# Performance work log

Hardware: AMD Instinct MI355X
Metric: run time of the kernel (lower is better)

## Reference

```python
import jax, jax.numpy as jnp
import numpy as np

NUM_HEADS = 8


def _forward(x, Wq, bq, Wk, bk, Wv, bv, Wo, bo, w1, b1, w2, b2, tau):
    B, S, E = x.shape
    H = NUM_HEADS
    hd = E // H
    scale = hd ** -0.5

    def heads(t):
        return t.reshape(B, S, H, hd).transpose(0, 2, 1, 3)  # [B,H,S,hd]

    q = heads(x @ Wq + bq)
    k = heads(x @ Wk + bk)
    v = heads(x @ Wv + bv)
    s = jnp.einsum('bhqd,bhkd->bhqk', q, k) * scale  # [B,H,S,S]

    # ---- autopoietic transform (vectorized over batch, no mask) ----
    s = jnp.clip(jnp.nan_to_num(s, nan=0.0, posinf=10.0, neginf=-10.0), -15.0, 15.0)
    ma = s.mean(axis=1)  # mean over heads -> [B,S,S]
    eps_safe = 0.05  # clamp(eps=1e-6, 0.05, 0.8)
    sa = jnp.clip(jnp.clip(ma, -8.0, 8.0) * eps_safe, -10.0, 10.0)
    # 1x1 conv on [1,1,S,S] == per-channel scalar scale+bias -> [B,C,S,S]
    hid = jax.nn.relu(jnp.clip(sa[:, None] * w1[None, :, None, None]
                               + b1[None, :, None, None], -5.0, 5.0))
    ap = jnp.clip(jnp.einsum('bcij,c->bij', hid, w2) + b2, -5.0, 5.0)
    taylor = jnp.clip(1.0 + 0.05 * (ap * 50.0), 0.5, 1.5)
    sig = jax.nn.sigmoid(taylor)
    p = jax.nn.softmax(jnp.clip(ma, -10.0, 10.0), axis=-1)
    Hent = -p * jnp.log(p + 1e-6)
    Fm = jax.nn.softmax(3.0 * Hent, axis=-1)
    t = sig * Fm
    eo = jnp.sqrt((ma * ma).sum(axis=(1, 2), keepdims=True)) + 1e-4  # fro norm
    et = jnp.sqrt((t * t).sum(axis=(1, 2), keepdims=True)) + 1e-4
    t = jnp.clip(eo / et, 0.8, 1.2) * t
    tm = t.mean(axis=(1, 2), keepdims=True)
    om = ma.mean(axis=(1, 2), keepdims=True)
    tstd = jnp.sqrt(jnp.clip(((t - tm) ** 2).mean(axis=(1, 2), keepdims=True), 0.01, None))
    ostd = jnp.sqrt(jnp.clip(((ma - om) ** 2).mean(axis=(1, 2), keepdims=True), 0.01, None))
    gd = jnp.clip(ostd / tstd, 0.8, 1.2)
    ar = jnp.clip(jnp.abs(ma).max(axis=(1, 2), keepdims=True), 1.0, 10.0)
    sm = jnp.clip(0.3 / jnp.log1p(ar), 0.1, 0.5)
    st = tm + sm * gd * (t - tm)  # scaled_transform
    ent = Hent.mean(axis=(1, 2), keepdims=True)
    ne = ent / jnp.log(jnp.float32(S))  # normalized entropy (max_entropy = log S)
    rr = 0.4 * (1.0 - jnp.clip(ne, 0.0, 0.4))  # residual ratio (base 0.4, entropy-damped)
    # blend transform back into per-head scores (res_scale = 1.0)
    s = s + rr[:, None] * (st - ma)[:, None]

    attn = jax.nn.softmax(s / tau, axis=-1)
    out = jnp.einsum('bhqk,bhkd->bhqd', attn, v)
    out = out.transpose(0, 2, 1, 3).reshape(B, S, E)
    return out @ Wo + bo


def setup_inputs() -> dict:
    key = jax.random.key(0)
    ks = jax.random.split(key, 8)
    B, S, E, C = 4, 512, 512, 128
    w_scale = 0.02
    return {
        'x': jax.random.normal(ks[0], (B, S, E), dtype=jnp.float32),
        'Wq': jax.random.normal(ks[1], (E, E), dtype=jnp.float32) * w_scale,
        'bq': jnp.zeros((E,), jnp.float32),
        'Wk': jax.random.normal(ks[2], (E, E), dtype=jnp.float32) * w_scale,
        'bk': jnp.zeros((E,), jnp.float32),
        'Wv': jax.random.normal(ks[3], (E, E), dtype=jnp.float32) * w_scale,
        'bv': jnp.zeros((E,), jnp.float32),
        'Wo': jax.random.normal(ks[4], (E, E), dtype=jnp.float32) * w_scale,
        'bo': jnp.zeros((E,), jnp.float32),
        'w1': jax.random.normal(ks[5], (C,), dtype=jnp.float32) * 0.5,
        'b1': jnp.zeros((C,), jnp.float32),
        'w2': jax.random.normal(ks[6], (C,), dtype=jnp.float32) * 0.1,
        'b2': jnp.zeros((1,), jnp.float32),
        'tau': jnp.ones((1,), jnp.float32),
    }


def reference(x, Wq, bq, Wk, bk, Wv, bv, Wo, bo, w1, b1, w2, b2, tau):
    return _forward(x, Wq, bq, Wk, bk, Wv, bv, Wo, bo, w1, b1, w2, b2, tau)
```

## Files before the change

### kernel.cpp

```cpp
#include <hip/hip_runtime.h>
#include <math.h>

#define BB 4
#define SS 512
#define EE 512
#define NH 8
#define HD 64
#define NC 128
#define NTAB 4096

typedef _Float16 f16x8 __attribute__((ext_vector_type(8)));
typedef float f32x4 __attribute__((ext_vector_type(4)));

struct HL { _Float16 h, l; };

__device__ __forceinline__ float clampf(float v, float lo, float hi) {
  return fminf(fmaxf(v, lo), hi);
}
__device__ __forceinline__ HL split16(float x) {
  HL r;
  r.h = (_Float16)x;
  r.l = (_Float16)(x - (float)r.h);
  return r;
}

__device__ __forceinline__ float waveRedSum(float v) {
#pragma unroll
  for (int o = 32; o; o >>= 1) v += __shfl_xor(v, o);
  return v;
}
__device__ __forceinline__ float waveRedMax(float v) {
#pragma unroll
  for (int o = 32; o; o >>= 1) v = fmaxf(v, __shfl_xor(v, o));
  return v;
}
__device__ __forceinline__ float blockRedSum8(float v, float* red) {
  int tid = threadIdx.x;
  v = waveRedSum(v);
  __syncthreads();
  if ((tid & 63) == 0) red[tid >> 6] = v;
  __syncthreads();
  float s = 0.f;
#pragma unroll
  for (int i = 0; i < 8; ++i) s += red[i];
  return s;
}
__device__ __forceinline__ float blockRedMax8(float v, float* red) {
  int tid = threadIdx.x;
  v = waveRedMax(v);
  __syncthreads();
  if ((tid & 63) == 0) red[tid >> 6] = v;
  __syncthreads();
  float s = red[0];
#pragma unroll
  for (int i = 1; i < 8; ++i) s = fmaxf(s, red[i]);
  return s;
}

__global__ __launch_bounds__(256) void k_prep(
    const float* __restrict__ Wq, const float* __restrict__ Wk,
    const float* __restrict__ Wv, const float* __restrict__ Wo,
    const float* __restrict__ x,
    _Float16* __restrict__ Wth, _Float16* __restrict__ Wtl,
    _Float16* __restrict__ xh) {
  const int j = blockIdx.x;
  const int tid = threadIdx.x;
  if (j >= 256) {
    const int rb = (j - 256) * 64;
    const int r = tid >> 2;
    const int c0 = (tid & 3) * 128;
    const float* src = x + (size_t)(rb + r) * EE + c0;
    _Float16* dst = xh + (size_t)(rb + r) * EE + c0;
#pragma unroll
    for (int c = 0; c < 128; c += 8) {
      float4 a = *(const float4*)(src + c);
      float4 b = *(const float4*)(src + c + 4);
      f16x8 h;
      h[0] = (_Float16)a.x; h[1] = (_Float16)a.y;
      h[2] = (_Float16)a.z; h[3] = (_Float16)a.w;
      h[4] = (_Float16)b.x; h[5] = (_Float16)b.y;
      h[6] = (_Float16)b.z; h[7] = (_Float16)b.w;
      *(f16x8*)(dst + c) = h;
    }
    return;
  }
  const int z = j >> 6;
  const int rem = j & 63;
  const int k0 = (rem & 7) * 64, n0 = (rem >> 3) * 64;
  const float* W = (z == 0) ? Wq : (z == 1) ? Wk : (z == 2) ? Wv : Wo;
  __shared__ float Tt[64][68];
  const int r = tid >> 2, c = (tid & 3) * 16;
#pragma unroll
  for (int jj = 0; jj < 16; jj += 4)
    *(float4*)&Tt[r][c + jj] =
        *(const float4*)(W + (size_t)(k0 + r) * EE + n0 + c + jj);
  __syncthreads();
  f16x8 h0, l0, h1, l1;
#pragma unroll
  for (int jj = 0; jj < 8; ++jj) {
    HL r0 = split16(Tt[c + jj][r]);
    HL r1 = split16(Tt[c + 8 + jj][r]);
    h0[jj] = r0.h; l0[jj] = r0.l;
    h1[jj] = r1.h; l1[jj] = r1.l;
  }
  _Float16* dh = Wth + ((size_t)z * EE + n0 + r) * EE + k0 + c;
  _Float16* dl = Wtl + ((size_t)z * EE + n0 + r) * EE + k0 + c;
  *(f16x8*)dh = h0;
  *(f16x8*)(dh + 8) = h1;
  *(f16x8*)dl = l0;
  *(f16x8*)(dl + 8) = l1;
}

__global__ __launch_bounds__(256) void k_qkv_mfma(
    const _Float16* __restrict__ xh,
    const _Float16* __restrict__ Wth, const _Float16* __restrict__ Wtl,
    const float* __restrict__ bq, const float* __restrict__ bk,
    const float* __restrict__ bv, const float* __restrict__ w1,
    const float* __restrict__ b1, const float* __restrict__ w2,
    const float* __restrict__ b2, float* __restrict__ T,
    _Float16* __restrict__ qh,
    _Float16* __restrict__ kh, _Float16* __restrict__ kl,
    _Float16* __restrict__ vth, _Float16* __restrict__ vtl) {
  const int which = blockIdx.z;
  const int tid = threadIdx.x;
  const int wave = tid >> 6, lane = tid & 63;
  const int quad = lane >> 4, l16 = lane & 15;
  const int m0 = blockIdx.y * 64;
  const int n0 = blockIdx.x * 64;
  const _Float16* Bh = Wth + (size_t)which * EE * EE;
  const _Float16* Bl = Wtl + (size_t)which * EE * EE;

  __shared__ __align__(16) char smpool[27648];
  _Float16(*LAh)[72] = (_Float16(*)[72])(smpool);
  _Float16(*LBh)[72] = (_Float16(*)[72])(smpool + 9216);
  _Float16(*LBl)[72] = (_Float16(*)[72])(smpool + 18432);
  float(*TR)[68] = (float(*)[68])(smpool);

  const int sr0 = tid >> 3, sc0 = (tid & 7) * 8;
  const int sr1 = sr0 + 32;

  f16x8 rA0h = *(const f16x8*)(xh + (size_t)(m0 + sr0) * EE + sc0);
  f16x8 rA1h = *(const f16x8*)(xh + (size_t)(m0 + sr1) * EE + sc0);
  f16x8 rB0h = *(const f16x8*)(Bh + (size_t)(n0 + sr0) * EE + sc0);
  f16x8 rB0l = *(const f16x8*)(Bl + (size_t)(n0 + sr0) * EE + sc0);
  f16x8 rB1h = *(const f16x8*)(Bh + (size_t)(n0 + sr1) * EE + sc0);
  f16x8 rB1l = *(const f16x8*)(Bl + (size_t)(n0 + sr1) * EE + sc0);

  f32x4 acc[4] = {};
  for (int k0 = 0; k0 < EE; k0 += 64) {
    if (k0) __syncthreads();
    *(f16x8*)&LAh[sr0][sc0] = rA0h;
    *(f16x8*)&LAh[sr1][sc0] = rA1h;
    *(f16x8*)&LBh[sr0][sc0] = rB0h;
    *(f16x8*)&LBl[sr0][sc0] = rB0l;
    *(f16x8*)&LBh[sr1][sc0] = rB1h;
    *(f16x8*)&LBl[sr1][sc0] = rB1l;
    __syncthreads();
    if (k0 + 64 < EE) {
      const int kn = k0 + 64;
      rA0h = *(const f16x8*)(xh + (size_t)(m0 + sr0) * EE + kn + sc0);
      rA1h = *(const f16x8*)(xh + (size_t)(m0 + sr1) * EE + kn + sc0);
      rB0h = *(const f16x8*)(Bh + (size_t)(n0 + sr0) * EE + kn + sc0);
      rB0l = *(const f16x8*)(Bl + (size_t)(n0 + sr0) * EE + kn + sc0);
      rB1h = *(const f16x8*)(Bh + (size_t)(n0 + sr1) * EE + kn + sc0);
      rB1l = *(const f16x8*)(Bl + (size_t)(n0 + sr1) * EE + kn + sc0);
    }
#pragma unroll
    for (int kk = 0; kk < 64; kk += 32) {
      f16x8 ah = *(const f16x8*)&LAh[wave * 16 + l16][kk + quad * 8];
#pragma unroll
      for (int nt = 0; nt < 4; ++nt) {
        f16x8 bhf = *(const f16x8*)&LBh[nt * 16 + l16][kk + quad * 8];
        f16x8 blf = *(const f16x8*)&LBl[nt * 16 + l16][kk + quad * 8];
        acc[nt] = __builtin_amdgcn_mfma_f32_16x16x32_f16(ah, bhf, acc[nt], 0, 0, 0);
        acc[nt] = __builtin_amdgcn_mfma_f32_16x16x32_f16(ah, blf, acc[nt], 0, 0, 0);
      }
    }
  }
  const float* bias = (which == 0) ? bq : (which == 1) ? bk : bv;
  if (which == 2) {
    __syncthreads();
#pragma unroll
    for (int nt = 0; nt < 4; ++nt) {
      const int dcol = nt * 16 + l16;
      const float bb = bias[n0 + nt * 16 + l16];
#pragma unroll
      for (int r = 0; r < 4; ++r)
        TR[dcol][wave * 16 + quad * 4 + r] = acc[nt][r] + bb;
    }
    __syncthreads();
    const int d = tid >> 2, cc = (tid & 3) * 16;
    const int bh = (m0 >> 9) * NH + (n0 >> 6);
    const int si0 = m0 & 511;
    f16x8 h0, l0, h1, l1;
#pragma unroll
    for (int jj = 0; jj < 8; ++jj) {
      HL r0 = split16(TR[d][cc + jj]);
      HL r1 = split16(TR[d][cc + 8 + jj]);
      h0[jj] = r0.h; l0[jj] = r0.l;
      h1[jj] = r1.h; l1[jj] = r1.l;
    }
    _Float16* dh = vth + ((size_t)bh * HD + d) * SS + si0 + cc;
    _Float16* dl = vtl + ((size_t)bh * HD + d) * SS + si0 + cc;
    *(f16x8*)dh = h0;
    *(f16x8*)(dh + 8) = h1;
    *(f16x8*)dl = l0;
    *(f16x8*)(dl + 8) = l1;
  } else {
    const float postscale = (which == 0) ? 0.125f : 1.0f;
    const int mbase = m0 + wave * 16 + quad * 4;
#pragma unroll
    for (int nt = 0; nt < 4; ++nt) {
      const int col = n0 + nt * 16 + l16;
      const float bb = bias[col];
#pragma unroll
      for (int r = 0; r < 4; ++r) {
        const size_t idx = (size_t)(mbase + r) * EE + col;
        const float val = (acc[nt][r] + bb) * postscale;
        if (which == 0) {
          qh[idx] = (_Float16)val;
        } else {
          HL sp = split16(val);
          kh[idx] = sp.h;
          kl[idx] = sp.l;
        }
      }
    }
    if (which == 0 && blockIdx.x == 0 && blockIdx.y < 17) {
      int idx = blockIdx.y * 256 + tid;
      if (idx <= NTAB) {
        float sa = -0.4f + (float)idx * (0.8f / (float)NTAB);
        float ap = 0.f;
#pragma unroll 4
        for (int c = 0; c < NC; ++c) {
          float h = fminf(fmaxf(sa * w1[c] + b1[c], 0.f), 5.f);
          ap += h * w2[c];
        }
        ap = clampf(ap + b2[0], -5.f, 5.f);
        float tay = clampf(1.0f + 0.05f * (ap * 50.0f), 0.5f, 1.5f);
        T[idx] = 1.0f / (1.0f + expf(-tay));
      }
    }
  }
}

__global__ __launch_bounds__(256) void k_ma_mfma(
    const _Float16* __restrict__ qh,
    const _Float16* __restrict__ kh, const _Float16* __restrict__ kl,
    _Float16* __restrict__ ma) {
  const int tid = threadIdx.x;
  const int wave = tid >> 6, lane = tid & 63;
  const int quad = lane >> 4, l16 = lane & 15;
  const int m0 = blockIdx.y * 64;
  const int n0 = blockIdx.x * 64;
  const _Float16* Bh = kh + (size_t)(m0 >> 9) * SS * EE;
  const _Float16* Bl = kl + (size_t)(m0 >> 9) * SS * EE;

  __shared__ _Float16 LAh[64][72], LBh[64][72], LBl[64][72];

  const int sr0 = tid >> 3, sc0 = (tid & 7) * 8;
  const int sr1 = sr0 + 32;

  f16x8 rA0h = *(const f16x8*)(qh + (size_t)(m0 + sr0) * EE + sc0);
  f16x8 rB0h = *(const f16x8*)(Bh + (size_t)(n0 + sr0) * EE + sc0);
  f16x8 rB0l = *(const f16x8*)(Bl + (size_t)(n0 + sr0) * EE + sc0);
  f16x8 rA1h = *(const f16x8*)(qh + (size_t)(m0 + sr1) * EE + sc0);
  f16x8 rB1h = *(const f16x8*)(Bh + (size_t)(n0 + sr1) * EE + sc0);
  f16x8 rB1l = *(const f16x8*)(Bl + (size_t)(n0 + sr1) * EE + sc0);

  f32x4 acc[4] = {};
  for (int k0 = 0; k0 < EE; k0 += 64) {
    if (k0) __syncthreads();
    *(f16x8*)&LAh[sr0][sc0] = rA0h;
    *(f16x8*)&LBh[sr0][sc0] = rB0h;
    *(f16x8*)&LBl[sr0][sc0] = rB0l;
    *(f16x8*)&LAh[sr1][sc0] = rA1h;
    *(f16x8*)&LBh[sr1][sc0] = rB1h;
    *(f16x8*)&LBl[sr1][sc0] = rB1l;
    __syncthreads();
    if (k0 + 64 < EE) {
      const int kn = k0 + 64;
      rA0h = *(const f16x8*)(qh + (size_t)(m0 + sr0) * EE + kn + sc0);
      rB0h = *(const f16x8*)(Bh + (size_t)(n0 + sr0) * EE + kn + sc0);
      rB0l = *(const f16x8*)(Bl + (size_t)(n0 + sr0) * EE + kn + sc0);
      rA1h = *(const f16x8*)(qh + (size_t)(m0 + sr1) * EE + kn + sc0);
      rB1h = *(const f16x8*)(Bh + (size_t)(n0 + sr1) * EE + kn + sc0);
      rB1l = *(const f16x8*)(Bl + (size_t)(n0 + sr1) * EE + kn + sc0);
    }
#pragma unroll
    for (int kk = 0; kk < 64; kk += 32) {
      f16x8 ah = *(const f16x8*)&LAh[wave * 16 + l16][kk + quad * 8];
#pragma unroll
      for (int nt = 0; nt < 4; ++nt) {
        f16x8 bhf = *(const f16x8*)&LBh[nt * 16 + l16][kk + quad * 8];
        f16x8 blf = *(const f16x8*)&LBl[nt * 16 + l16][kk + quad * 8];
        acc[nt] = __builtin_amdgcn_mfma_f32_16x16x32_f16(ah, bhf, acc[nt], 0, 0, 0);
        acc[nt] = __builtin_amdgcn_mfma_f32_16x16x32_f16(ah, blf, acc[nt], 0, 0, 0);
      }
    }
  }
  const int mbase = m0 + wave * 16 + quad * 4;
#pragma unroll
  for (int nt = 0; nt < 4; ++nt) {
    const int col = n0 + nt * 16 + l16;
#pragma unroll
    for (int r = 0; r < 4; ++r) {
      ma[(size_t)(mbase + r) * SS + col] = (_Float16)(acc[nt][r] * 0.125f);
    }
  }
}

__global__ __launch_bounds__(256) void k_rowstat(
    const _Float16* __restrict__ ma, const float* __restrict__ T,
    _Float16* __restrict__ t_un, float* __restrict__ rowred) {
  const int row = blockIdx.x * 4 + (threadIdx.x >> 6);
  const int lane = threadIdx.x & 63;

  f16x8 mv8 = *(const f16x8*)(ma + (size_t)row * SS + lane * 8);
  float m[8];
#pragma unroll
  for (int e = 0; e < 8; ++e) m[e] = (float)mv8[e];

  float sma = 0.f, sma2 = 0.f, mabs = 0.f;
#pragma unroll
  for (int e = 0; e < 8; ++e) {
    sma += m[e];
    sma2 += m[e] * m[e];
    mabs = fmaxf(mabs, fabsf(m[e]));
  }
  sma = waveRedSum(sma);
  sma2 = waveRedSum(sma2);
  mabs = waveRedMax(mabs);

  float ex[8], esum = 0.f;
#pragma unroll
  for (int e = 0; e < 8; ++e) {
    ex[e] = __expf(clampf(m[e], -10.f, 10.f));
    esum += ex[e];
  }
  esum = waveRedSum(esum);
  float inv = 1.0f / esum;
  float Hv[8], sH = 0.f;
#pragma unroll
  for (int e = 0; e < 8; ++e) {
    float pp = ex[e] * inv;
    Hv[e] = -pp * __logf(pp + 1e-6f);
    sH += Hv[e];
  }
  sH = waveRedSum(sH);

  float fx[8], fsum = 0.f;
#pragma unroll
  for (int e = 0; e < 8; ++e) {
    fx[e] = __expf(3.0f * Hv[e]);
    fsum += fx[e];
  }
  fsum = waveRedSum(fsum);
  float finv = 1.0f / fsum;

  float t[8], st = 0.f, st2 = 0.f;
#pragma unroll
  for (int e = 0; e < 8; ++e) {
    float sa = clampf(m[e], -8.f, 8.f) * 0.05f;
    float pos = (sa + 0.4f) * ((float)NTAB / 0.8f);
    int idx = (int)pos;
    idx = idx < 0 ? 0 : (idx > NTAB - 1 ? NTAB - 1 : idx);
    float frac = pos - (float)idx;
    float g0 = T[idx], g1 = T[idx + 1];
    float sig = g0 + (g1 - g0) * frac;
    t[e] = sig * fx[e] * finv;
    st += t[e];
    st2 += t[e] * t[e];
  }
  st = waveRedSum(st);
  st2 = waveRedSum(st2);
  {
    f16x8 tw;
#pragma unroll
    for (int e = 0; e < 8; ++e) tw[e] = (_Float16)t[e];
    *(f16x8*)(t_un + (size_t)row * SS + lane * 8) = tw;
  }
  if (lane == 0) {
    float* rp = rowred + (size_t)row * 8;
    rp[0] = sma; rp[1] = sma2; rp[2] = mabs;
    rp[3] = st;  rp[4] = st2;  rp[5] = sH;
  }
}

__global__ __launch_bounds__(512) void k_av_fused(
    const _Float16* __restrict__ qh,
    const _Float16* __restrict__ kh, const _Float16* __restrict__ kl,
    const _Float16* __restrict__ ma, const _Float16* __restrict__ t_un,
    const float* __restrict__ rowred, const float* __restrict__ tau,
    const _Float16* __restrict__ vth, const _Float16* __restrict__ vtl,
    _Float16* __restrict__ oh) {
  const int bh = blockIdx.y;
  const int b_ = bh >> 3, hh = bh & 7;
  const int m0 = blockIdx.x * 64;
  const int tid = threadIdx.x;
  const int wave = tid >> 6, lane = tid & 63;
  const int quad = lane >> 4, l16 = lane & 15;
  const int g = wave >> 1, h2 = wave & 1;

  __shared__ float red[8];
  float c0, c1, c2;
  {
    const float* rp = rowred + ((size_t)b_ * SS + tid) * 8;
    float sma = blockRedSum8(rp[0], red);
    float sma2 = blockRedSum8(rp[1], red);
    float mabs = blockRedMax8(rp[2], red);
    float st = blockRedSum8(rp[3], red);
    float st2 = blockRedSum8(rp[4], red);
    float sH = blockRedSum8(rp[5], red);
    const float N = (float)(SS * SS);
    float eo = sqrtf(sma2) + 1e-4f;
    float et = sqrtf(st2) + 1e-4f;
    float r = clampf(eo / et, 0.8f, 1.2f);
    float tmean = r * st / N;
    float om = sma / N;
    float vart = r * r * fmaxf(st2 / N - (st / N) * (st / N), 0.f);
    float tstd = sqrtf(fmaxf(vart, 0.01f));
    float varo = fmaxf(sma2 / N - om * om, 0.f);
    float ostd = sqrtf(fmaxf(varo, 0.01f));
    float gd = clampf(ostd / tstd, 0.8f, 1.2f);
    float ar = clampf(mabs, 1.f, 10.f);
    float sm = clampf(0.3f / log1pf(ar), 0.1f, 0.5f);
    float ent = sH / N;
    float ne = ent / logf((float)SS);
    float rr = 0.4f * (1.f - clampf(ne, 0.f, 0.4f));
    float G = sm * gd;
    c0 = rr * (1.f - G) * tmean;
    c1 = rr * G * r;
    c2 = rr;
  }
  const float itau = 1.0f / tau[0];

  __shared__ _Float16 Ph[64][40];
  __shared__ float Zp[64][2];

  const size_t qbase = (size_t)(b_ * SS + m0 + g * 16 + l16) * EE + hh * HD;
  f16x8 a_hi[2];
#pragma unroll
  for (int ks = 0; ks < 2; ++ks)
    a_hi[ks] = *(const f16x8*)(qh + qbase + ks * 32 + quad * 8);

  const size_t kbase = (size_t)b_ * SS * EE + hh * HD;
  const size_t vbase = ((size_t)bh * HD + g * 16 + l16) * SS;
  const size_t mb0 =
      (size_t)(b_ * SS + m0 + g * 16 + quad * 4) * SS + h2 * 16 + l16;

  f16x8 kb_h[2], kb_l[2], vb_h, vb_l;
  _Float16 mv[4], tv[4];
  {
    const size_t kr = kbase + (size_t)(h2 * 16 + l16) * EE;
#pragma unroll
    for (int ks = 0; ks < 2; ++ks) {
      kb_h[ks] = *(const f16x8*)(kh + kr + ks * 32 + quad * 8);
      kb_l[ks] = *(const f16x8*)(kl + kr + ks * 32 + quad * 8);
    }
    vb_h = *(const f16x8*)(vth + vbase + quad * 8);
    vb_l = *(const f16x8*)(vtl + vbase + quad * 8);
#pragma unroll
    for (int r = 0; r < 4; ++r) {
      mv[r] = ma[mb0 + (size_t)r * SS];
      tv[r] = t_un[mb0 + (size_t)r * SS];
    }
  }

  float z[4] = {0.f, 0.f, 0.f, 0.f};
  f32x4 oacc[2] = {};
  for (int k0 = 0; k0 < SS; k0 += 32) {
    f32x4 qacc = {};
#pragma unroll
    for (int ks = 0; ks < 2; ++ks) {
      qacc = __builtin_amdgcn_mfma_f32_16x16x32_f16(a_hi[ks], kb_h[ks], qacc, 0, 0, 0);
      qacc = __builtin_amdgcn_mfma_f32_16x16x32_f16(a_hi[ks], kb_l[ks], qacc, 0, 0, 0);
    }
    const f16x8 vh_c = vb_h, vl_c = vb_l;
    __syncthreads();
#pragma unroll
    for (int r = 0; r < 4; ++r) {
      float sc = clampf(qacc[r], -15.f, 15.f);
      float v = (sc + c0 + c1 * (float)tv[r] - c2 * (float)mv[r]) * itau;
      float e = __expf(v) * 1.52587890625e-05f;
      z[r] += e;
      Ph[g * 16 + quad * 4 + r][h2 * 16 + l16] = (_Float16)e;
    }
    if (k0 + 32 < SS) {
      const int kn = k0 + 32;
      const size_t kr = kbase + (size_t)(kn + h2 * 16 + l16) * EE;
#pragma unroll
      for (int ks = 0; ks < 2; ++ks) {
        kb_h[ks] = *(const f16x8*)(kh + kr + ks * 32 + quad * 8);
        kb_l[ks] = *(const f16x8*)(kl + kr + ks * 32 + quad * 8);
      }
      vb_h = *(const f16x8*)(vth + vbase + kn + quad * 8);
      vb_l = *(const f16x8*)(vtl + vbase + kn + quad * 8);
#pragma unroll
      for (int r = 0; r < 4; ++r) {
        mv[r] = ma[mb0 + (size_t)r * SS + kn];
        tv[r] = t_un[mb0 + (size_t)r * SS + kn];
      }
    }
    __syncthreads();
#pragma unroll
    for (int e2 = 0; e2 < 2; ++e2) {
      const int mt2 = h2 * 2 + e2;
      f16x8 ah = *(const f16x8*)&Ph[mt2 * 16 + l16][quad * 8];
      oacc[e2] = __builtin_amdgcn_mfma_f32_16x16x32_f16(ah, vh_c, oacc[e2], 0, 0, 0);
      oacc[e2] = __builtin_amdgcn_mfma_f32_16x16x32_f16(ah, vl_c, oacc[e2], 0, 0, 0);
    }
  }
#pragma unroll
  for (int off = 1; off < 16; off <<= 1) {
#pragma unroll
    for (int r = 0; r < 4; ++r) z[r] += __shfl_xor(z[r], off);
  }
  if (l16 == 0) {
#pragma unroll
    for (int r = 0; r < 4; ++r) Zp[g * 16 + quad * 4 + r][h2] = z[r];
  }
  __syncthreads();
#pragma unroll
  for (int e2 = 0; e2 < 2; ++e2) {
    const int mt2 = h2 * 2 + e2;
#pragma unroll
    for (int r = 0; r < 4; ++r) {
      const int lr = mt2 * 16 + quad * 4 + r;
      const float Z = Zp[lr][0] + Zp[lr][1];
      const float oV = oacc[e2][r] / Z;
      const int si = m0 + lr;
      const size_t idx =
          ((size_t)(b_ * SS + si)) * EE + hh * HD + g * 16 + l16;
      oh[idx] = (_Float16)oV;
    }
  }
}

__global__ __launch_bounds__(256) void k_out_mfma(
    const _Float16* __restrict__ oh,
    const _Float16* __restrict__ Wth, const _Float16* __restrict__ Wtl,
    const float* __restrict__ bo, float* __restrict__ out) {
  const int tid = threadIdx.x;
  const int wave = tid >> 6, lane = tid & 63;
  const int quad = lane >> 4, l16 = lane & 15;
  const int m0 = blockIdx.y * 64;
  const int n0 = blockIdx.x * 64;
  const _Float16* Bh = Wth + (size_t)3 * EE * EE;
  const _Float16* Bl = Wtl + (size_t)3 * EE * EE;

  __shared__ _Float16 LAh[64][72], LBh[64][72], LBl[64][72];

  const int sr0 = tid >> 3, sc0 = (tid & 7) * 8;
  const int sr1 = sr0 + 32;

  f16x8 rA0h = *(const f16x8*)(oh + (size_t)(m0 + sr0) * EE + sc0);
  f16x8 rB0h = *(const f16x8*)(Bh + (size_t)(n0 + sr0) * EE + sc0);
  f16x8 rB0l = *(const f16x8*)(Bl + (size_t)(n0 + sr0) * EE + sc0);
  f16x8 rA1h = *(const f16x8*)(oh + (size_t)(m0 + sr1) * EE + sc0);
  f16x8 rB1h = *(const f16x8*)(Bh + (size_t)(n0 + sr1) * EE + sc0);
  f16x8 rB1l = *(const f16x8*)(Bl + (size_t)(n0 + sr1) * EE + sc0);

  f32x4 acc[4] = {};
  for (int k0 = 0; k0 < EE; k0 += 64) {
    if (k0) __syncthreads();
    *(f16x8*)&LAh[sr0][sc0] = rA0h;
    *(f16x8*)&LBh[sr0][sc0] = rB0h;
    *(f16x8*)&LBl[sr0][sc0] = rB0l;
    *(f16x8*)&LAh[sr1][sc0] = rA1h;
    *(f16x8*)&LBh[sr1][sc0] = rB1h;
    *(f16x8*)&LBl[sr1][sc0] = rB1l;
    __syncthreads();
    if (k0 + 64 < EE) {
      const int kn = k0 + 64;
      rA0h = *(const f16x8*)(oh + (size_t)(m0 + sr0) * EE + kn + sc0);
      rB0h = *(const f16x8*)(Bh + (size_t)(n0 + sr0) * EE + kn + sc0);
      rB0l = *(const f16x8*)(Bl + (size_t)(n0 + sr0) * EE + kn + sc0);
      rA1h = *(const f16x8*)(oh + (size_t)(m0 + sr1) * EE + kn + sc0);
      rB1h = *(const f16x8*)(Bh + (size_t)(n0 + sr1) * EE + kn + sc0);
      rB1l = *(const f16x8*)(Bl + (size_t)(n0 + sr1) * EE + kn + sc0);
    }
#pragma unroll
    for (int kk = 0; kk < 64; kk += 32) {
      f16x8 ah = *(const f16x8*)&LAh[wave * 16 + l16][kk + quad * 8];
#pragma unroll
      for (int nt = 0; nt < 4; ++nt) {
        f16x8 bhf = *(const f16x8*)&LBh[nt * 16 + l16][kk + quad * 8];
        f16x8 blf = *(const f16x8*)&LBl[nt * 16 + l16][kk + quad * 8];
        acc[nt] = __builtin_amdgcn_mfma_f32_16x16x32_f16(ah, bhf, acc[nt], 0, 0, 0);
        acc[nt] = __builtin_amdgcn_mfma_f32_16x16x32_f16(ah, blf, acc[nt], 0, 0, 0);
      }
    }
  }
  const int mbase = m0 + wave * 16 + quad * 4;
#pragma unroll
  for (int nt = 0; nt < 4; ++nt) {
    const int col = n0 + nt * 16 + l16;
    const float bb = bo[col];
#pragma unroll
    for (int r = 0; r < 4; ++r) {
      const int m = mbase + r;
      out[(size_t)m * EE + col] = acc[nt][r] + bb;
    }
  }
}

extern "C" void kernel_launch(void* const* d_in, const int* in_sizes, int n_in,
                              void* d_out, int out_size, void* d_ws,
                              size_t ws_size, hipStream_t stream) {
  const float* x = (const float*)d_in[0];
  const float* Wq = (const float*)d_in[1];
  const float* bq = (const float*)d_in[2];
  const float* Wk = (const float*)d_in[3];
  const float* bk = (const float*)d_in[4];
  const float* Wv = (const float*)d_in[5];
  const float* bv = (const float*)d_in[6];
  const float* Wo = (const float*)d_in[7];
  const float* bo = (const float*)d_in[8];
  const float* w1 = (const float*)d_in[9];
  const float* b1 = (const float*)d_in[10];
  const float* w2 = (const float*)d_in[11];
  const float* b2 = (const float*)d_in[12];
  const float* tau = (const float*)d_in[13];
  float* out = (float*)d_out;

  const size_t NX = (size_t)2048 * EE;
  const size_t NW = (size_t)4 * EE * EE;
  const size_t NQK = (size_t)BB * SS * EE;
  const size_t NSS = (size_t)BB * SS * SS;

  _Float16* Wth = (_Float16*)d_ws;
  _Float16* Wtl = Wth + NW;
  _Float16* xh = Wtl + NW;
  _Float16* qh = xh + NX;
  _Float16* kh = qh + NQK;
  _Float16* kl = kh + NQK;
  _Float16* vth = kl + NQK;
  _Float16* vtl = vth + NQK;
  _Float16* oh = vtl + NQK;
  _Float16* ma = oh + NX;
  _Float16* t_un = ma + NSS;
  float* T = (float*)(t_un + NSS);
  float* rowred = T + 8192;

  k_prep<<<288, 256, 0, stream>>>(Wq, Wk, Wv, Wo, x, Wth, Wtl, xh);
  k_qkv_mfma<<<dim3(8, 32, 3), 256, 0, stream>>>(xh, Wth, Wtl, bq, bk, bv, w1,
                                                 b1, w2, b2, T, qh, kh, kl,
                                                 vth, vtl);
  k_ma_mfma<<<dim3(8, 32), 256, 0, stream>>>(qh, kh, kl, ma);
  k_rowstat<<<512, 256, 0, stream>>>(ma, T, t_un, rowred);
  k_av_fused<<<dim3(8, 32), 512, 0, stream>>>(qh, kh, kl, ma, t_un,
                                              rowred, tau, vth, vtl, oh);
  k_out_mfma<<<dim3(8, 32), 256, 0, stream>>>(oh, Wth, Wtl, bo, out);
}
```

Before: 165.1 us.

## Split attention-value kernel over key halves and merge partials in output GEMM

```diff
diff --git a/kernel.cpp b/kernel.cpp
--- a/kernel.cpp
+++ b/kernel.cpp
@@ -34,27 +34,21 @@
   for (int o = 32; o; o >>= 1) v = fmaxf(v, __shfl_xor(v, o));
   return v;
 }
-__device__ __forceinline__ float blockRedSum8(float v, float* red) {
+__device__ __forceinline__ float blockRedSum(float v, float* red) {
   int tid = threadIdx.x;
   v = waveRedSum(v);
   __syncthreads();
   if ((tid & 63) == 0) red[tid >> 6] = v;
   __syncthreads();
-  float s = 0.f;
-#pragma unroll
-  for (int i = 0; i < 8; ++i) s += red[i];
-  return s;
-}
-__device__ __forceinline__ float blockRedMax8(float v, float* red) {
+  return red[0] + red[1] + red[2] + red[3];
+}
+__device__ __forceinline__ float blockRedMax(float v, float* red) {
   int tid = threadIdx.x;
   v = waveRedMax(v);
   __syncthreads();
   if ((tid & 63) == 0) red[tid >> 6] = v;
   __syncthreads();
-  float s = red[0];
-#pragma unroll
-  for (int i = 1; i < 8; ++i) s = fmaxf(s, red[i]);
-  return s;
+  return fmaxf(fmaxf(red[0], red[1]), fmaxf(red[2], red[3]));
 }
 
 __global__ __launch_bounds__(256) void k_prep(
@@ -387,31 +381,20 @@
   }
 }
 
-__global__ __launch_bounds__(512) void k_av_fused(
-    const _Float16* __restrict__ qh,
-    const _Float16* __restrict__ kh, const _Float16* __restrict__ kl,
-    const _Float16* __restrict__ ma, const _Float16* __restrict__ t_un,
-    const float* __restrict__ rowred, const float* __restrict__ tau,
-    const _Float16* __restrict__ vth, const _Float16* __restrict__ vtl,
-    _Float16* __restrict__ oh) {
-  const int bh = blockIdx.y;
-  const int b_ = bh >> 3, hh = bh & 7;
-  const int m0 = blockIdx.x * 64;
+__global__ __launch_bounds__(256) void k_consts(
+    const float* __restrict__ rowred, float* __restrict__ cvec) {
+  const int b_ = blockIdx.x;
   const int tid = threadIdx.x;
-  const int wave = tid >> 6, lane = tid & 63;
-  const int quad = lane >> 4, l16 = lane & 15;
-  const int g = wave >> 1, h2 = wave & 1;
-
-  __shared__ float red[8];
-  float c0, c1, c2;
-  {
-    const float* rp = rowred + ((size_t)b_ * SS + tid) * 8;
-    float sma = blockRedSum8(rp[0], red);
-    float sma2 = blockRedSum8(rp[1], red);
-    float mabs = blockRedMax8(rp[2], red);
-    float st = blockRedSum8(rp[3], red);
-    float st2 = blockRedSum8(rp[4], red);
-    float sH = blockRedSum8(rp[5], red);
+  __shared__ float red[4];
+  const float* r0 = rowred + ((size_t)b_ * SS + tid * 2) * 8;
+  const float* r1 = r0 + 8;
+  float sma = blockRedSum(r0[0] + r1[0], red);
+  float sma2 = blockRedSum(r0[1] + r1[1], red);
+  float mabs = blockRedMax(fmaxf(r0[2], r1[2]), red);
+  float st = blockRedSum(r0[3] + r1[3], red);
+  float st2 = blockRedSum(r0[4] + r1[4], red);
+  float sH = blockRedSum(r0[5] + r1[5], red);
+  if (tid == 0) {
     const float N = (float)(SS * SS);
     float eo = sqrtf(sma2) + 1e-4f;
     float et = sqrtf(st2) + 1e-4f;
@@ -429,52 +412,74 @@
     float ne = ent / logf((float)SS);
     float rr = 0.4f * (1.f - clampf(ne, 0.f, 0.4f));
     float G = sm * gd;
-    c0 = rr * (1.f - G) * tmean;
-    c1 = rr * G * r;
-    c2 = rr;
-  }
+    cvec[b_ * 4 + 0] = rr * (1.f - G) * tmean;
+    cvec[b_ * 4 + 1] = rr * G * r;
+    cvec[b_ * 4 + 2] = rr;
+  }
+}
+
+__global__ __launch_bounds__(256) void k_av_split(
+    const _Float16* __restrict__ qh,
+    const _Float16* __restrict__ kh, const _Float16* __restrict__ kl,
+    const _Float16* __restrict__ ma, const _Float16* __restrict__ t_un,
+    const float* __restrict__ cvec, const float* __restrict__ tau,
+    const _Float16* __restrict__ vth, const _Float16* __restrict__ vtl,
+    float* __restrict__ o_part, float* __restrict__ z_part) {
+  const int bh = blockIdx.y;
+  const int b_ = bh >> 3, hh = bh & 7;
+  const int m0 = blockIdx.x * 32;
+  const int ksp = blockIdx.z;
+  const int kbeg = ksp * 256, kend = kbeg + 256;
+  const int tid = threadIdx.x;
+  const int wave = tid >> 6, lane = tid & 63;
+  const int quad = lane >> 4, l16 = lane & 15;
+  const int mt = wave >> 1, nt = wave & 1;
+
+  const float c0 = cvec[b_ * 4 + 0];
+  const float c1 = cvec[b_ * 4 + 1];
+  const float c2 = cvec[b_ * 4 + 2];
   const float itau = 1.0f / tau[0];
 
-  __shared__ _Float16 Ph[64][40];
-  __shared__ float Zp[64][2];
-
-  const size_t qbase = (size_t)(b_ * SS + m0 + g * 16 + l16) * EE + hh * HD;
+  __shared__ _Float16 Ph[32][40];
+  __shared__ float Zp[32][2];
+
+  const size_t qbase = (size_t)(b_ * SS + m0 + mt * 16 + l16) * EE + hh * HD;
   f16x8 a_hi[2];
 #pragma unroll
-  for (int ks = 0; ks < 2; ++ks)
-    a_hi[ks] = *(const f16x8*)(qh + qbase + ks * 32 + quad * 8);
+  for (int s2 = 0; s2 < 2; ++s2)
+    a_hi[s2] = *(const f16x8*)(qh + qbase + s2 * 32 + quad * 8);
 
   const size_t kbase = (size_t)b_ * SS * EE + hh * HD;
-  const size_t vbase = ((size_t)bh * HD + g * 16 + l16) * SS;
+  const size_t vbase = ((size_t)bh * HD + wave * 16 + l16) * SS;
   const size_t mb0 =
-      (size_t)(b_ * SS + m0 + g * 16 + quad * 4) * SS + h2 * 16 + l16;
+      (size_t)(b_ * SS + m0 + mt * 16 + quad * 4) * SS + nt * 16 + l16;
 
   f16x8 kb_h[2], kb_l[2], vb_h, vb_l;
   _Float16 mv[4], tv[4];
   {
-    const size_t kr = kbase + (size_t)(h2 * 16 + l16) * EE;
-#pragma unroll
-    for (int ks = 0; ks < 2; ++ks) {
-      kb_h[ks] = *(const f16x8*)(kh + kr + ks * 32 + quad * 8);
-      kb_l[ks] = *(const f16x8*)(kl + kr + ks * 32 + quad * 8);
-    }
-    vb_h = *(const f16x8*)(vth + vbase + quad * 8);
-    vb_l = *(const f16x8*)(vtl + vbase + quad * 8);
+    const size_t kr = kbase + (size_t)(kbeg + nt * 16 + l16) * EE;
+#pragma unroll
+    for (int s2 = 0; s2 < 2; ++s2) {
+      kb_h[s2] = *(const f16x8*)(kh + kr + s2 * 32 + quad * 8);
+      kb_l[s2] = *(const f16x8*)(kl + kr + s2 * 32 + quad * 8);
+    }
+    vb_h = *(const f16x8*)(vth + vbase + kbeg + quad * 8);
+    vb_l = *(const f16x8*)(vtl + vbase + kbeg + quad * 8);
 #pragma unroll
     for (int r = 0; r < 4; ++r) {
-      mv[r] = ma[mb0 + (size_t)r * SS];
-      tv[r] = t_un[mb0 + (size_t)r * SS];
+      mv[r] = ma[mb0 + (size_t)r * SS + kbeg];
+      tv[r] = t_un[mb0 + (size_t)r * SS + kbeg];
     }
   }
 
   float z[4] = {0.f, 0.f, 0.f, 0.f};
   f32x4 oacc[2] = {};
-  for (int k0 = 0; k0 < SS; k0 += 32) {
+  for (int k0 = kbeg; k0 < kend; k0 += 32) {
     f32x4 qacc = {};
 #pragma unroll
-    for (int ks = 0; ks < 2; ++ks) {
-      qacc = __builtin_amdgcn_mfma_f32_16x16x32_f16(a_hi[ks], kb_h[ks], qacc, 0, 0, 0);
-      qacc = __builtin_amdgcn_mfma_f32_16x16x32_f16(a_hi[ks], kb_l[ks], qacc, 0, 0, 0);
+    for (int s2 = 0; s2 < 2; ++s2) {
+      qacc = __builtin_amdgcn_mfma_f32_16x16x32_f16(a_hi[s2], kb_h[s2], qacc, 0, 0, 0);
+      qacc = __builtin_amdgcn_mfma_f32_16x16x32_f16(a_hi[s2], kb_l[s2], qacc, 0, 0, 0);
     }
     const f16x8 vh_c = vb_h, vl_c = vb_l;
     __syncthreads();
@@ -484,15 +489,15 @@
       float v = (sc + c0 + c1 * (float)tv[r] - c2 * (float)mv[r]) * itau;
       float e = __expf(v) * 1.52587890625e-05f;
       z[r] += e;
-      Ph[g * 16 + quad * 4 + r][h2 * 16 + l16] = (_Float16)e;
-    }
-    if (k0 + 32 < SS) {
+      Ph[mt * 16 + quad * 4 + r][nt * 16 + l16] = (_Float16)e;
+    }
+    if (k0 + 32 < kend) {
       const int kn = k0 + 32;
-      const size_t kr = kbase + (size_t)(kn + h2 * 16 + l16) * EE;
-#pragma unroll
-      for (int ks = 0; ks < 2; ++ks) {
-        kb_h[ks] = *(const f16x8*)(kh + kr + ks * 32 + quad * 8);
-        kb_l[ks] = *(const f16x8*)(kl + kr + ks * 32 + quad * 8);
+      const size_t kr = kbase + (size_t)(kn + nt * 16 + l16) * EE;
+#pragma unroll
+      for (int s2 = 0; s2 < 2; ++s2) {
+        kb_h[s2] = *(const f16x8*)(kh + kr + s2 * 32 + quad * 8);
+        kb_l[s2] = *(const f16x8*)(kl + kr + s2 * 32 + quad * 8);
       }
       vb_h = *(const f16x8*)(vth + vbase + kn + quad * 8);
       vb_l = *(const f16x8*)(vtl + vbase + kn + quad * 8);
@@ -504,11 +509,10 @@
     }
     __syncthreads();
 #pragma unroll
-    for (int e2 = 0; e2 < 2; ++e2) {
-      const int mt2 = h2 * 2 + e2;
+    for (int mt2 = 0; mt2 < 2; ++mt2) {
       f16x8 ah = *(const f16x8*)&Ph[mt2 * 16 + l16][quad * 8];
-      oacc[e2] = __builtin_amdgcn_mfma_f32_16x16x32_f16(ah, vh_c, oacc[e2], 0, 0, 0);
-      oacc[e2] = __builtin_amdgcn_mfma_f32_16x16x32_f16(ah, vl_c, oacc[e2], 0, 0, 0);
+      oacc[mt2] = __builtin_amdgcn_mfma_f32_16x16x32_f16(ah, vh_c, oacc[mt2], 0, 0, 0);
+      oacc[mt2] = __builtin_amdgcn_mfma_f32_16x16x32_f16(ah, vl_c, oacc[mt2], 0, 0, 0);
     }
   }
 #pragma unroll
@@ -518,27 +522,30 @@
   }
   if (l16 == 0) {
 #pragma unroll
-    for (int r = 0; r < 4; ++r) Zp[g * 16 + quad * 4 + r][h2] = z[r];
+    for (int r = 0; r < 4; ++r) Zp[mt * 16 + quad * 4 + r][nt] = z[r];
   }
   __syncthreads();
-#pragma unroll
-  for (int e2 = 0; e2 < 2; ++e2) {
-    const int mt2 = h2 * 2 + e2;
+  float* op = o_part + (size_t)ksp * (2048 * EE);
+  if (tid < 32) {
+    z_part[(size_t)ksp * (2048 * NH) + ((size_t)(b_ * SS + m0 + tid)) * NH + hh] =
+        Zp[tid][0] + Zp[tid][1];
+  }
+#pragma unroll
+  for (int mt2 = 0; mt2 < 2; ++mt2) {
 #pragma unroll
     for (int r = 0; r < 4; ++r) {
       const int lr = mt2 * 16 + quad * 4 + r;
-      const float Z = Zp[lr][0] + Zp[lr][1];
-      const float oV = oacc[e2][r] / Z;
       const int si = m0 + lr;
       const size_t idx =
-          ((size_t)(b_ * SS + si)) * EE + hh * HD + g * 16 + l16;
-      oh[idx] = (_Float16)oV;
+          ((size_t)(b_ * SS + si)) * EE + hh * HD + wave * 16 + l16;
+      op[idx] = oacc[mt2][r];
     }
   }
 }
 
 __global__ __launch_bounds__(256) void k_out_mfma(
-    const _Float16* __restrict__ oh,
+    const float* __restrict__ o0, const float* __restrict__ o1,
+    const float* __restrict__ z0, const float* __restrict__ z1,
     const _Float16* __restrict__ Wth, const _Float16* __restrict__ Wtl,
     const float* __restrict__ bo, float* __restrict__ out) {
   const int tid = threadIdx.x;
@@ -554,29 +561,59 @@
   const int sr0 = tid >> 3, sc0 = (tid & 7) * 8;
   const int sr1 = sr0 + 32;
 
-  f16x8 rA0h = *(const f16x8*)(oh + (size_t)(m0 + sr0) * EE + sc0);
+  float4 pa0, pa1, pb0, pb1, qa0, qa1, qb0, qb1;
+  float pz, qz;
+  {
+    const size_t off0 = (size_t)(m0 + sr0) * EE + sc0;
+    const size_t off1 = (size_t)(m0 + sr1) * EE + sc0;
+    pa0 = *(const float4*)(o0 + off0); pa1 = *(const float4*)(o0 + off0 + 4);
+    pb0 = *(const float4*)(o1 + off0); pb1 = *(const float4*)(o1 + off0 + 4);
+    qa0 = *(const float4*)(o0 + off1); qa1 = *(const float4*)(o0 + off1 + 4);
+    qb0 = *(const float4*)(o1 + off1); qb1 = *(const float4*)(o1 + off1 + 4);
+    pz = z0[(size_t)(m0 + sr0) * NH] + z1[(size_t)(m0 + sr0) * NH];
+    qz = z0[(size_t)(m0 + sr1) * NH] + z1[(size_t)(m0 + sr1) * NH];
+  }
   f16x8 rB0h = *(const f16x8*)(Bh + (size_t)(n0 + sr0) * EE + sc0);
   f16x8 rB0l = *(const f16x8*)(Bl + (size_t)(n0 + sr0) * EE + sc0);
-  f16x8 rA1h = *(const f16x8*)(oh + (size_t)(m0 + sr1) * EE + sc0);
   f16x8 rB1h = *(const f16x8*)(Bh + (size_t)(n0 + sr1) * EE + sc0);
   f16x8 rB1l = *(const f16x8*)(Bl + (size_t)(n0 + sr1) * EE + sc0);
 
   f32x4 acc[4] = {};
   for (int k0 = 0; k0 < EE; k0 += 64) {
     if (k0) __syncthreads();
-    *(f16x8*)&LAh[sr0][sc0] = rA0h;
+    {
+      float rz0 = 1.0f / pz, rz1 = 1.0f / qz;
+      float a0[8] = {pa0.x + pb0.x, pa0.y + pb0.y, pa0.z + pb0.z, pa0.w + pb0.w,
+                     pa1.x + pb1.x, pa1.y + pb1.y, pa1.z + pb1.z, pa1.w + pb1.w};
+      float a1[8] = {qa0.x + qb0.x, qa0.y + qb0.y, qa0.z + qb0.z, qa0.w + qb0.w,
+                     qa1.x + qb1.x, qa1.y + qb1.y, qa1.z + qb1.z, qa1.w + qb1.w};
+      f16x8 h0, h1;
+#pragma unroll
+      for (int j = 0; j < 8; ++j) {
+        h0[j] = (_Float16)(a0[j] * rz0);
+        h1[j] = (_Float16)(a1[j] * rz1);
+      }
+      *(f16x8*)&LAh[sr0][sc0] = h0;
+      *(f16x8*)&LAh[sr1][sc0] = h1;
+    }
     *(f16x8*)&LBh[sr0][sc0] = rB0h;
     *(f16x8*)&LBl[sr0][sc0] = rB0l;
-    *(f16x8*)&LAh[sr1][sc0] = rA1h;
     *(f16x8*)&LBh[sr1][sc0] = rB1h;
     *(f16x8*)&LBl[sr1][sc0] = rB1l;
     __syncthreads();
     if (k0 + 64 < EE) {
       const int kn = k0 + 64;
-      rA0h = *(const f16x8*)(oh + (size_t)(m0 + sr0) * EE + kn + sc0);
+      const int hd2 = kn >> 6;
+      const size_t off0 = (size_t)(m0 + sr0) * EE + kn + sc0;
+      const size_t off1 = (size_t)(m0 + sr1) * EE + kn + sc0;
+      pa0 = *(const float4*)(o0 + off0); pa1 = *(const float4*)(o0 + off0 + 4);
+      pb0 = *(const float4*)(o1 + off0); pb1 = *(const float4*)(o1 + off0 + 4);
+      qa0 = *(const float4*)(o0 + off1); qa1 = *(const float4*)(o0 + off1 + 4);
+      qb0 = *(const float4*)(o1 + off1); qb1 = *(const float4*)(o1 + off1 + 4);
+      pz = z0[(size_t)(m0 + sr0) * NH + hd2] + z1[(size_t)(m0 + sr0) * NH + hd2];
+      qz = z0[(size_t)(m0 + sr1) * NH + hd2] + z1[(size_t)(m0 + sr1) * NH + hd2];
       rB0h = *(const f16x8*)(Bh + (size_t)(n0 + sr0) * EE + kn + sc0);
       rB0l = *(const f16x8*)(Bl + (size_t)(n0 + sr0) * EE + kn + sc0);
-      rA1h = *(const f16x8*)(oh + (size_t)(m0 + sr1) * EE + kn + sc0);
       rB1h = *(const f16x8*)(Bh + (size_t)(n0 + sr1) * EE + kn + sc0);
       rB1l = *(const f16x8*)(Bl + (size_t)(n0 + sr1) * EE + kn + sc0);
     }
@@ -637,11 +674,13 @@
   _Float16* kl = kh + NQK;
   _Float16* vth = kl + NQK;
   _Float16* vtl = vth + NQK;
-  _Float16* oh = vtl + NQK;
-  _Float16* ma = oh + NX;
+  _Float16* ma = vtl + NQK;
   _Float16* t_un = ma + NSS;
   float* T = (float*)(t_un + NSS);
   float* rowred = T + 8192;
+  float* cvec = rowred + 2048 * 8;
+  float* o_part = cvec + 16;
+  float* z_part = o_part + 2 * NX;
 
   k_prep<<<288, 256, 0, stream>>>(Wq, Wk, Wv, Wo, x, Wth, Wtl, xh);
   k_qkv_mfma<<<dim3(8, 32, 3), 256, 0, stream>>>(xh, Wth, Wtl, bq, bk, bv, w1,
@@ -649,7 +688,10 @@
                                                  vth, vtl);
   k_ma_mfma<<<dim3(8, 32), 256, 0, stream>>>(qh, kh, kl, ma);
   k_rowstat<<<512, 256, 0, stream>>>(ma, T, t_un, rowred);
-  k_av_fused<<<dim3(8, 32), 512, 0, stream>>>(qh, kh, kl, ma, t_un,
-                                              rowred, tau, vth, vtl, oh);
-  k_out_mfma<<<dim3(8, 32), 256, 0, stream>>>(oh, Wth, Wtl, bo, out);
-}
+  k_consts<<<4, 256, 0, stream>>>(rowred, cvec);
+  k_av_split<<<dim3(16, 32, 2), 256, 0, stream>>>(
+      qh, kh, kl, ma, t_un, cvec, tau, vth, vtl, o_part, z_part);
+  k_out_mfma<<<dim3(8, 32), 256, 0, stream>>>(o_part, o_part + NX, z_part,
+                                              z_part + 2048 * NH, Wth, Wtl, bo,
+                                              out);
+}
```

Measured after the change: 171.9 us. 4.1% more time.
